# Kernel tuning notes

Hardware: AMD Instinct MI355X
Metric: run time of the kernel (lower is better)

## Reference

```python
import jax, jax.numpy as jnp
import numpy as np
from jax import lax

T, B, S = 64, 32, 64
V, E, H = 32000, 512, 512

def _p(key, shape, scale=0.05):
    return (jax.random.normal(key, shape, dtype=jnp.float32) * scale)

def setup_inputs() -> dict:
    key = jax.random.key(0)
    ks = jax.random.split(key, 24)
    inp = {
        'trg': jax.random.randint(ks[0], (T, B), 0, V),
        'encoded_src': jax.random.normal(ks[1], (S, B, 2 * H), dtype=jnp.float32),
        'emb': _p(ks[2], (V, E)),
        # LSTM layer 0: input = E + 2H
        'W_ih0': _p(ks[3], (4 * H, E + 2 * H)), 'W_hh0': _p(ks[4], (4 * H, H)),
        'b_ih0': _p(ks[5], (4 * H,)), 'b_hh0': _p(ks[6], (4 * H,)),
        # LSTM layer 1: input = H
        'W_ih1': _p(ks[7], (4 * H, H)), 'W_hh1': _p(ks[8], (4 * H, H)),
        'b_ih1': _p(ks[9], (4 * H,)), 'b_hh1': _p(ks[10], (4 * H,)),
        # attn_annot: 2H -> H
        'Wa': _p(ks[11], (H, 2 * H)), 'ba': _p(ks[12], (H,)),
        # attn_hidden: H -> H
        'Wh': _p(ks[13], (H, H)), 'bh': _p(ks[14], (H,)),
        # other: H -> 1
        'Wo': _p(ks[15], (1, H)), 'bo': _p(ks[16], (1,)),
        # penult: 3H -> E
        'Wp': _p(ks[17], (E, 3 * H)), 'bp': _p(ks[18], (E,)),
        # out bias (weight tied to emb)
        'b_out': _p(ks[19], (V,)),
    }
    return inp

def _lstm_cell(x, h, c, W_ih, W_hh, b_ih, b_hh):
    # PyTorch gate order: i, f, g, o
    g = x @ W_ih.T + b_ih + h @ W_hh.T + b_hh
    i, f, gg, o = jnp.split(g, 4, axis=-1)
    c_new = jax.nn.sigmoid(f) * c + jax.nn.sigmoid(i) * jnp.tanh(gg)
    h_new = jax.nn.sigmoid(o) * jnp.tanh(c_new)
    return h_new, c_new

def reference(trg, encoded_src, emb, W_ih0, W_hh0, b_ih0, b_hh0,
              W_ih1, W_hh1, b_ih1, b_hh1, Wa, ba, Wh, bh, Wo, bo,
              Wp, bp, b_out):
    trg_emb = emb[trg]                                # [T,B,E]
    annot_scores = encoded_src @ Wa.T + ba            # [S,B,H]
    Hd = W_hh0.shape[1]
    Bd = encoded_src.shape[1]
    h0 = jnp.zeros((2, Bd, Hd), dtype=encoded_src.dtype)
    c0 = jnp.zeros((2, Bd, Hd), dtype=encoded_src.dtype)
    ctx0 = jnp.zeros((Bd, encoded_src.shape[2]), dtype=encoded_src.dtype)

    def step(carry, emb_t):
        h, c, ctx = carry
        x = jnp.concatenate([emb_t, ctx], axis=1)      # [B, E+2H]
        h0n, c0n = _lstm_cell(x,   h[0], c[0], W_ih0, W_hh0, b_ih0, b_hh0)
        h1n, c1n = _lstm_cell(h0n, h[1], c[1], W_ih1, W_hh1, b_ih1, b_hh1)
        out = h1n                                      # [B,H]
        hs = out @ Wh.T + bh                           # [B,H]
        e = jnp.tanh(hs[None] + annot_scores) @ Wo.T + bo   # [S,B,1]
        a = jax.nn.softmax(e, axis=0)[..., 0]          # [S,B]
        ctx_new = jnp.einsum('sb,sbd->bd', a, encoded_src)  # [B,2H]
        stacked = jnp.concatenate([out, ctx_new], axis=1)   # [B,3H]
        return (jnp.stack([h0n, h1n]), jnp.stack([c0n, c1n]), ctx_new), stacked

    (h, c, _), all_scores = lax.scan(step, (h0, c0, ctx0), trg_emb)  # all_scores [T,B,3H]
    pen = all_scores @ Wp.T + bp                       # [T,B,E]
    logits = pen @ emb.T + b_out                       # [T,B,V] (tied weights)
    scores = jax.nn.log_softmax(logits, axis=2)
    return (scores, h, c)
```

## Files before the change

### kernel.cpp

```cpp
#include <hip/hip_runtime.h>


typedef unsigned short u16;
typedef short bf16x8 __attribute__((ext_vector_type(8)));
typedef float f32x4 __attribute__((ext_vector_type(4)));

#define MFMA_BF16(a, b, c) __builtin_amdgcn_mfma_f32_16x16x32_bf16((a), (b), (c), 0, 0, 0)

struct __attribute__((aligned(8))) U16x4 { u16 x, y, z, w; };

__device__ __forceinline__ float b2f(u16 u) {
  unsigned v = ((unsigned)u) << 16; float f; __builtin_memcpy(&f, &v, 4); return f;
}
__device__ __forceinline__ u16 f2b(float f) {
  unsigned u; __builtin_memcpy(&u, &f, 4);
  u = (u + 0x7FFFu + ((u >> 16) & 1u)) >> 16;
  return (u16)u;
}
__device__ __forceinline__ float sigm(float x) { return 1.f / (1.f + __expf(-x)); }
__device__ __forceinline__ float tanh_fast(float x) {
  x = fminf(fmaxf(x, -15.f), 15.f);
  float e = __expf(2.f * x);
  return (e - 1.f) / (e + 1.f);
}

__device__ __forceinline__ bf16x8 bl16(const u16* p) {
  bf16x8 v;
  asm volatile("global_load_dwordx4 %0, %1, off sc0 sc1" : "=v"(v) : "v"(p) : "memory");
  return v;
}
__device__ __forceinline__ float blf(const float* p) {
  float v;
  asm volatile("global_load_dword %0, %1, off sc0 sc1" : "=v"(v) : "v"(p) : "memory");
  return v;
}
__device__ __forceinline__ u16 blu16(const u16* p) {
  unsigned v;
  asm volatile("global_load_ushort %0, %1, off sc0 sc1" : "=v"(v) : "v"(p) : "memory");
  return (u16)v;
}
__device__ __forceinline__ void bs16(u16* p, u16 d) {
  unsigned dd = d;
  asm volatile("global_store_short %0, %1, off sc0 sc1" :: "v"(p), "v"(dd) : "memory");
}
__device__ __forceinline__ void bs32(float* p, float d) {
  asm volatile("global_store_dword %0, %1, off sc0 sc1" :: "v"(p), "v"(d) : "memory");
}
__device__ __forceinline__ void bs32u(u16* p, unsigned d) {
  asm volatile("global_store_dword %0, %1, off sc0 sc1" :: "v"(p), "v"(d) : "memory");
}
__device__ __forceinline__ void vmwait() {
  asm volatile("s_waitcnt vmcnt(0)" ::: "memory");
  __builtin_amdgcn_sched_barrier(0);
}

__global__ void f2b4_kernel(const float* __restrict__ src, u16* __restrict__ dst, long n4) {
  long i = (long)blockIdx.x * blockDim.x + threadIdx.x;
  long stride = (long)gridDim.x * blockDim.x;
  for (; i < n4; i += stride) {
    float4 v = ((const float4*)src)[i];
    U16x4 o; o.x = f2b(v.x); o.y = f2b(v.y); o.z = f2b(v.z); o.w = f2b(v.w);
    ((U16x4*)dst)[i] = o;
  }
}

__global__ void f2b4_strided(const float* __restrict__ src, u16* __restrict__ dst,
                             int rows, int cols4, int sld, int soff, int dld, int doff) {
  int total = rows * cols4;
  for (int i = blockIdx.x * blockDim.x + threadIdx.x; i < total; i += gridDim.x * blockDim.x) {
    int r = i / cols4, c4 = i - r * cols4;
    float4 v = *(const float4*)(src + (size_t)r * sld + soff + c4 * 4);
    U16x4 o; o.x = f2b(v.x); o.y = f2b(v.y); o.z = f2b(v.z); o.w = f2b(v.w);
    *(U16x4*)(dst + (size_t)r * dld + doff + c4 * 4) = o;
  }
}

__global__ void gather_emb_kernel(const int* __restrict__ trg, const float* __restrict__ emb,
                                  u16* __restrict__ out) {
  int r = blockIdx.x;
  int v = trg[r];
  const float* srow = emb + (size_t)v * 512;
  u16* drow = out + (size_t)r * 512;
  for (int e = threadIdx.x; e < 128; e += blockDim.x) {
    float4 x = ((const float4*)srow)[e];
    U16x4 o; o.x = f2b(x.x); o.y = f2b(x.y); o.z = f2b(x.z); o.w = f2b(x.w);
    ((U16x4*)drow)[e] = o;
  }
}

__global__ void annot_tr_kernel(const float* __restrict__ annot, u16* __restrict__ abt) {
  int b = blockIdx.x >> 6, s = blockIdx.x & 63;
  const float* src = annot + (size_t)(s * 32 + b) * 512;
  u16* dst = abt + (size_t)(b * 64 + s) * 512;
  int j = threadIdx.x;
  float4 v = ((const float4*)src)[j];
  U16x4 o; o.x = f2b(v.x); o.y = f2b(v.y); o.z = f2b(v.z); o.w = f2b(v.w);
  ((U16x4*)dst)[j] = o;
}

__global__ void enc_tr_kernel(const float* __restrict__ enc, u16* __restrict__ ebt) {
  int b = blockIdx.x >> 6, s = blockIdx.x & 63;
  const float* src = enc + (size_t)(s * 32 + b) * 1024;
  u16* dst = ebt + (size_t)(b * 64 + s) * 1024;
  int j = threadIdx.x;
  float4 v = ((const float4*)src)[j];
  U16x4 o; o.x = f2b(v.x); o.y = f2b(v.y); o.z = f2b(v.z); o.w = f2b(v.w);
  ((U16x4*)dst)[j] = o;
}

template <int MODE>
__global__ __launch_bounds__(256) void gemm_bt(
    const u16* __restrict__ A, const u16* __restrict__ B,
    float* __restrict__ outF, u16* __restrict__ outB,
    const float* __restrict__ bias0, const float* __restrict__ bias1,
    int N, int K, int ntiles, float* __restrict__ pmax, float* __restrict__ psum) {
  const int l = threadIdx.x & 63, wv = threadIdx.x >> 6;
  const int m0 = blockIdx.x * 128 + wv * 32;
  const int n0 = blockIdx.y * 64;
  const int kg = ((l >> 4) << 3);
  const u16* Ap0 = A + (size_t)(m0 + (l & 15)) * K + kg;
  const u16* Ap1 = Ap0 + (size_t)16 * K;
  const u16* Bp = B + (size_t)(n0 + (l & 15)) * K + kg;
  f32x4 acc[2][4] = {};
  for (int k0 = 0; k0 < K; k0 += 32) {
    bf16x8 a0 = *(const bf16x8*)(Ap0 + k0);
    bf16x8 a1 = *(const bf16x8*)(Ap1 + k0);
#pragma unroll
    for (int nf = 0; nf < 4; ++nf) {
      bf16x8 bb = *(const bf16x8*)(Bp + (size_t)(nf * 16) * K + k0);
      acc[0][nf] = MFMA_BF16(a0, bb, acc[0][nf]);
      acc[1][nf] = MFMA_BF16(a1, bb, acc[1][nf]);
    }
  }
  float biasv[4];
#pragma unroll
  for (int nf = 0; nf < 4; ++nf) {
    int col = n0 + nf * 16 + (l & 15);
    float bv = bias0 ? bias0[col] : 0.f;
    if (bias1) bv += bias1[col];
    biasv[nf] = bv;
  }
#pragma unroll
  for (int mi = 0; mi < 2; ++mi)
#pragma unroll
    for (int nf = 0; nf < 4; ++nf)
#pragma unroll
      for (int i = 0; i < 4; ++i) acc[mi][nf][i] += biasv[nf];

#pragma unroll
  for (int mi = 0; mi < 2; ++mi)
#pragma unroll
    for (int i = 0; i < 4; ++i) {
      int row = m0 + mi * 16 + ((l >> 4) << 2) + i;
#pragma unroll
      for (int nf = 0; nf < 4; ++nf) {
        int col = n0 + nf * 16 + (l & 15);
        if constexpr (MODE == 1)
          outB[(size_t)row * N + col] = f2b(acc[mi][nf][i]);
        else
          outF[(size_t)row * N + col] = acc[mi][nf][i];
      }
    }
  if constexpr (MODE == 2) {
    float lm[2][4], se[2][4];
#pragma unroll
    for (int mi = 0; mi < 2; ++mi)
#pragma unroll
      for (int i = 0; i < 4; ++i) {
        float m_ = acc[mi][0][i];
#pragma unroll
        for (int nf = 1; nf < 4; ++nf) m_ = fmaxf(m_, acc[mi][nf][i]);
        lm[mi][i] = m_;
      }
#pragma unroll
    for (int d = 1; d < 16; d <<= 1)
#pragma unroll
      for (int mi = 0; mi < 2; ++mi)
#pragma unroll
        for (int i = 0; i < 4; ++i) lm[mi][i] = fmaxf(lm[mi][i], __shfl_xor(lm[mi][i], d));
#pragma unroll
    for (int mi = 0; mi < 2; ++mi)
#pragma unroll
      for (int i = 0; i < 4; ++i) {
        float s_ = 0.f;
#pragma unroll
        for (int nf = 0; nf < 4; ++nf) s_ += __expf(acc[mi][nf][i] - lm[mi][i]);
        se[mi][i] = s_;
      }
#pragma unroll
    for (int d = 1; d < 16; d <<= 1)
#pragma unroll
      for (int mi = 0; mi < 2; ++mi)
#pragma unroll
        for (int i = 0; i < 4; ++i) se[mi][i] += __shfl_xor(se[mi][i], d);
    if ((l & 15) == 0) {
#pragma unroll
      for (int mi = 0; mi < 2; ++mi)
#pragma unroll
        for (int i = 0; i < 4; ++i) {
          int row = m0 + mi * 16 + ((l >> 4) << 2) + i;
          pmax[(size_t)row * ntiles + blockIdx.y] = lm[mi][i];
          psum[(size_t)row * ntiles + blockIdx.y] = se[mi][i];
        }
    }
  }
}

__device__ __forceinline__ void grid_barrier(unsigned* flags, unsigned phase) {
  __syncthreads();
  if (threadIdx.x == 0) {
    __hip_atomic_store(flags + blockIdx.x * 32, phase, __ATOMIC_RELAXED,
                       __HIP_MEMORY_SCOPE_AGENT);
  }
  if (threadIdx.x < 32) {
    int spins = 0;
    while (__hip_atomic_load(flags + threadIdx.x * 32, __ATOMIC_RELAXED,
                             __HIP_MEMORY_SCOPE_AGENT) < phase &&
           spins < 2000000) ++spins;
  }
  __syncthreads();
}

__global__ __launch_bounds__(512, 2) void scan_kernel(
    const u16* __restrict__ xW0,
    const u16* __restrict__ Wcat0,
    const u16* __restrict__ Wcat1,
    const u16* __restrict__ Whb,
    const float* __restrict__ b_ih1, const float* __restrict__ b_hh1,
    const float* __restrict__ bh, const float* __restrict__ Wo, const float* __restrict__ bo,
    const u16* __restrict__ annot_bt,
    const u16* __restrict__ enc_bt,
    u16* __restrict__ ctxb,
    u16* __restrict__ h0b,
    u16* __restrict__ h1b,
    float* __restrict__ c0, float* __restrict__ c1,
    float* __restrict__ hs,
    u16* __restrict__ scoresb,
    float* __restrict__ dout_hc,
    unsigned* __restrict__ flags) {
  __shared__ float sm[16384];
  const int w = blockIdx.x;
  const int tid = threadIdx.x;
  const int l = tid & 63, wv = tid >> 6;
  const int jh0 = w * 16;
  const int bE = tid >> 4, jlE = tid & 15;
  unsigned phase = 0;

  float gb1[4];
#pragma unroll
  for (int g = 0; g < 4; ++g) gb1[g] = b_ih1[g * 512 + jh0 + jlE] + b_hh1[g * 512 + jh0 + jlE];
  const float bhv = bh[jh0 + jlE];
  const float bov = bo[0];

  for (int t = 0; t < 64; ++t) {
    const int pA = t & 1;
    {
      const int kg = ((l >> 4) << 3);
      u16 xw[4];
      {
        const u16* xp = xW0 + (size_t)(t * 32 + bE) * 2048 + jh0 + jlE;
#pragma unroll
        for (int g = 0; g < 4; ++g) xw[g] = blu16(xp + g * 512);
      }
      bf16x8 a0[6], a1[6];
#pragma unroll
      for (int kk = 0; kk < 6; ++kk) {
        const int k0 = wv * 192 + kk * 32;
        const u16* ab; int ld, off;
        if (k0 < 1024) { ab = ctxb; ld = 1024; off = k0; }
        else { ab = h0b + pA * 32 * 512; ld = 512; off = k0 - 1024; }
        a0[kk] = bl16(ab + (size_t)(l & 15) * ld + off + kg);
        a1[kk] = bl16(ab + (size_t)((l & 15) + 16) * ld + off + kg);
      }
      vmwait();
      f32x4 acc[2][4] = {};
#pragma unroll
      for (int kk = 0; kk < 6; ++kk) {
        const int k0 = wv * 192 + kk * 32;
#pragma unroll
        for (int g = 0; g < 4; ++g) {
          bf16x8 bb = *(const bf16x8*)(Wcat0 + (size_t)(g * 512 + jh0 + (l & 15)) * 1536 + k0 + kg);
          acc[0][g] = MFMA_BF16(a0[kk], bb, acc[0][g]);
          acc[1][g] = MFMA_BF16(a1[kk], bb, acc[1][g]);
        }
      }
#pragma unroll
      for (int mi = 0; mi < 2; ++mi)
#pragma unroll
        for (int g = 0; g < 4; ++g)
#pragma unroll
          for (int i = 0; i < 4; ++i) {
            int m = mi * 16 + ((l >> 4) << 2) + i;
            sm[(wv * 32 + m) * 64 + g * 16 + (l & 15)] = acc[mi][g][i];
          }
      __syncthreads();
      {
        const int b = bE, jl = jlE, jh = jh0 + jl;
        float gate[4];
#pragma unroll
        for (int g = 0; g < 4; ++g) {
          float s = 0.f;
#pragma unroll
          for (int kv = 0; kv < 8; ++kv) s += sm[(kv * 32 + b) * 64 + g * 16 + jl];
          gate[g] = s + b2f(xw[g]);
        }
        float cn = sigm(gate[1]) * c0[b * 512 + jh] + sigm(gate[0]) * tanh_fast(gate[2]);
        float hn = sigm(gate[3]) * tanh_fast(cn);
        c0[b * 512 + jh] = cn;
        bs16(h0b + (pA ^ 1) * 32 * 512 + b * 512 + jh, f2b(hn));
        if (t == 63) { dout_hc[b * 512 + jh] = hn; dout_hc[32768 + b * 512 + jh] = cn; }
      }
    }
    grid_barrier(flags, ++phase);
    {
      const int kg = ((l >> 4) << 3);
      bf16x8 a0[4], a1[4];
#pragma unroll
      for (int kk = 0; kk < 4; ++kk) {
        const int k0 = wv * 128 + kk * 32;
        const u16* ab; int off;
        if (k0 < 512) { ab = h0b + (pA ^ 1) * 32 * 512; off = k0; }
        else { ab = h1b + pA * 32 * 512; off = k0 - 512; }
        a0[kk] = bl16(ab + (size_t)(l & 15) * 512 + off + kg);
        a1[kk] = bl16(ab + (size_t)((l & 15) + 16) * 512 + off + kg);
      }
      vmwait();
      f32x4 acc[2][4] = {};
#pragma unroll
      for (int kk = 0; kk < 4; ++kk) {
        const int k0 = wv * 128 + kk * 32;
#pragma unroll
        for (int g = 0; g < 4; ++g) {
          bf16x8 bb = *(const bf16x8*)(Wcat1 + (size_t)(g * 512 + jh0 + (l & 15)) * 1024 + k0 + kg);
          acc[0][g] = MFMA_BF16(a0[kk], bb, acc[0][g]);
          acc[1][g] = MFMA_BF16(a1[kk], bb, acc[1][g]);
        }
      }
#pragma unroll
      for (int mi = 0; mi < 2; ++mi)
#pragma unroll
        for (int g = 0; g < 4; ++g)
#pragma unroll
          for (int i = 0; i < 4; ++i) {
            int m = mi * 16 + ((l >> 4) << 2) + i;
            sm[(wv * 32 + m) * 64 + g * 16 + (l & 15)] = acc[mi][g][i];
          }
      __syncthreads();
      {
        const int b = bE, jl = jlE, jh = jh0 + jl;
        float gate[4];
#pragma unroll
        for (int g = 0; g < 4; ++g) {
          float s = 0.f;
#pragma unroll
          for (int kv = 0; kv < 8; ++kv) s += sm[(kv * 32 + b) * 64 + g * 16 + jl];
          gate[g] = s + gb1[g];
        }
        float cn = sigm(gate[1]) * c1[b * 512 + jh] + sigm(gate[0]) * tanh_fast(gate[2]);
        float hn = sigm(gate[3]) * tanh_fast(cn);
        c1[b * 512 + jh] = cn;
        u16 hb = f2b(hn);
        bs16(h1b + (pA ^ 1) * 32 * 512 + b * 512 + jh, hb);
        bs16(scoresb + (size_t)(t * 32 + b) * 1536 + jh, hb);
        if (t == 63) { dout_hc[16384 + b * 512 + jh] = hn; dout_hc[32768 + 16384 + b * 512 + jh] = cn; }
      }
    }
    grid_barrier(flags, ++phase);
    {
      const int kg = ((l >> 4) << 3);
      const u16* h1n = h1b + (pA ^ 1) * 32 * 512;
      bf16x8 a0[2], a1[2];
#pragma unroll
      for (int kk = 0; kk < 2; ++kk) {
        const int k0 = wv * 64 + kk * 32;
        a0[kk] = bl16(h1n + (size_t)(l & 15) * 512 + k0 + kg);
        a1[kk] = bl16(h1n + (size_t)((l & 15) + 16) * 512 + k0 + kg);
      }
      vmwait();
      f32x4 acc2[2] = {};
#pragma unroll
      for (int kk = 0; kk < 2; ++kk) {
        const int k0 = wv * 64 + kk * 32;
        bf16x8 bb = *(const bf16x8*)(Whb + (size_t)(jh0 + (l & 15)) * 512 + k0 + kg);
        acc2[0] = MFMA_BF16(a0[kk], bb, acc2[0]);
        acc2[1] = MFMA_BF16(a1[kk], bb, acc2[1]);
      }
#pragma unroll
      for (int mi = 0; mi < 2; ++mi)
#pragma unroll
        for (int i = 0; i < 4; ++i)
          sm[(wv * 32 + mi * 16 + ((l >> 4) << 2) + i) * 16 + (l & 15)] = acc2[mi][i];
      __syncthreads();
      {
        const int b = bE, jl = jlE;
        float s = 0.f;
#pragma unroll
        for (int kv = 0; kv < 8; ++kv) s += sm[(kv * 32 + b) * 16 + jl];
        bs32(hs + b * 512 + jh0 + jl, s + bhv);
      }
    }
    grid_barrier(flags, ++phase);
    {
      const int b = w;
      float* hs_s = sm;
      float* wo_s = sm + 512;
      float* red = sm + 1024;
      float* a_s = sm + 1536;
      float hv = blf(hs + b * 512 + tid);
      float wov = Wo[tid];
      vmwait();
      hs_s[tid] = hv;
      wo_s[tid] = wov;
      __syncthreads();
      const int s_ = tid >> 3, ks = tid & 7;
      const u16* arow = annot_bt + (size_t)(b * 64 + s_) * 512 + ks * 64;
      float accv = 0.f;
#pragma unroll
      for (int kk8 = 0; kk8 < 8; ++kk8) {
        bf16x8 av = *(const bf16x8*)(arow + kk8 * 8);
#pragma unroll
        for (int j = 0; j < 8; ++j) {
          int k = ks * 64 + kk8 * 8 + j;
          accv += tanh_fast(hs_s[k] + b2f((u16)av[j])) * wo_s[k];
        }
      }
      red[tid] = accv;
      __syncthreads();
      if (tid < 64) {
        float e = bov;
#pragma unroll
        for (int j = 0; j < 8; ++j) e += red[tid * 8 + j];
        float mx = e;
#pragma unroll
        for (int d = 1; d < 64; d <<= 1) mx = fmaxf(mx, __shfl_xor(mx, d));
        float p = __expf(e - mx);
        float ss = p;
#pragma unroll
        for (int d = 1; d < 64; d <<= 1) ss += __shfl_xor(ss, d);
        a_s[tid] = p / ss;
      }
      __syncthreads();
      float cx0 = 0.f, cx1 = 0.f;
      const u16* erow = enc_bt + (size_t)b * 65536 + tid * 2;
#pragma unroll 8
      for (int s2 = 0; s2 < 64; ++s2) {
        unsigned ev = *(const unsigned*)(erow + (size_t)s2 * 1024);
        float av = a_s[s2];
        cx0 += av * b2f((u16)(ev & 0xFFFFu));
        cx1 += av * b2f((u16)(ev >> 16));
      }
      u16 u0 = f2b(cx0), u1 = f2b(cx1);
      unsigned pk = (unsigned)u0 | ((unsigned)u1 << 16);
      bs32u(ctxb + b * 1024 + tid * 2, pk);
      bs32u(scoresb + (size_t)(t * 32 + b) * 1536 + 512 + tid * 2, pk);
    }
    grid_barrier(flags, ++phase);
  }
}

__global__ __launch_bounds__(256) void lse_kernel(const float* __restrict__ pmax,
                                                  const float* __restrict__ psum,
                                                  float* __restrict__ lse, int nt) {
  __shared__ float red[256];
  const int r = blockIdx.x;
  float m = -3.4e38f;
  for (int j = threadIdx.x; j < nt; j += 256) m = fmaxf(m, pmax[(size_t)r * nt + j]);
  red[threadIdx.x] = m; __syncthreads();
  for (int s = 128; s > 0; s >>= 1) {
    if (threadIdx.x < s) red[threadIdx.x] = fmaxf(red[threadIdx.x], red[threadIdx.x + s]);
    __syncthreads();
  }
  const float M = red[0]; __syncthreads();
  float s_ = 0.f;
  for (int j = threadIdx.x; j < nt; j += 256)
    s_ += psum[(size_t)r * nt + j] * __expf(pmax[(size_t)r * nt + j] - M);
  red[threadIdx.x] = s_; __syncthreads();
  for (int s = 128; s > 0; s >>= 1) {
    if (threadIdx.x < s) red[threadIdx.x] += red[threadIdx.x + s];
    __syncthreads();
  }
  if (threadIdx.x == 0) lse[r] = M + logf(red[0]);
}

__global__ void finalize_kernel(float* __restrict__ out, const float* __restrict__ lse) {
  const long n4 = 16384000;
  for (long i = (long)blockIdx.x * blockDim.x + threadIdx.x; i < n4;
       i += (long)gridDim.x * blockDim.x) {
    float4 v = ((float4*)out)[i];
    float L = lse[i / 8000];
    v.x -= L; v.y -= L; v.z -= L; v.w -= L;
    ((float4*)out)[i] = v;
  }
}

extern "C" void kernel_launch(void* const* d_in, const int* in_sizes, int n_in,
                              void* d_out, int out_size, void* d_ws, size_t ws_size,
                              hipStream_t stream) {
  const int* trg = (const int*)d_in[0];
  const float* enc = (const float*)d_in[1];
  const float* emb = (const float*)d_in[2];
  const float* W_ih0 = (const float*)d_in[3];
  const float* W_hh0 = (const float*)d_in[4];
  const float* b_ih0 = (const float*)d_in[5];
  const float* b_hh0 = (const float*)d_in[6];
  const float* W_ih1 = (const float*)d_in[7];
  const float* W_hh1 = (const float*)d_in[8];
  const float* b_ih1 = (const float*)d_in[9];
  const float* b_hh1 = (const float*)d_in[10];
  const float* Wa = (const float*)d_in[11];
  const float* ba = (const float*)d_in[12];
  const float* Wh = (const float*)d_in[13];
  const float* bh = (const float*)d_in[14];
  const float* Wo = (const float*)d_in[15];
  const float* bo = (const float*)d_in[16];
  const float* Wp = (const float*)d_in[17];
  const float* bp = (const float*)d_in[18];
  const float* b_out = (const float*)d_in[19];
  float* out = (float*)d_out;

  unsigned char* ws = (unsigned char*)d_ws;
  size_t off = 0;
  auto alloc = [&](size_t bytes) -> void* {
    void* p = ws + off; off += (bytes + 255) & ~(size_t)255; return p;
  };
  u16* emb_b = (u16*)alloc(32768000);
  u16* trgemb_b = (u16*)alloc(2097152);
  u16* enc_b = (u16*)alloc(4194304);
  u16* Wemb0_b = (u16*)alloc(2097152);
  u16* Wcat0_b = (u16*)alloc(6291456);
  u16* Wcat1_b = (u16*)alloc(4194304);
  u16* Wa_b = (u16*)alloc(1048576);
  u16* Wh_b = (u16*)alloc(524288);
  u16* Wp_b = (u16*)alloc(1572864);
  u16* xW0_b = (u16*)alloc(8388608);
  float* annot = (float*)alloc(4194304);
  u16* scoresb = (u16*)alloc(6291456);
  u16* pen_b = (u16*)alloc(2097152);
  u16* ctxb = (u16*)alloc(65536);
  u16* h0b = (u16*)alloc(65536);
  u16* h1b = (u16*)alloc(65536);
  float* c0 = (float*)alloc(65536);
  float* c1 = (float*)alloc(65536);
  float* hsbuf = (float*)alloc(65536);
  float* pmax = (float*)alloc(4194304);
  float* psum = (float*)alloc(4194304);
  float* lse = (float*)alloc(8192);
  unsigned* flags = (unsigned*)alloc(4096);
  if (off > ws_size) return;

  u16* annot_bt = (u16*)pmax;
  u16* enc_bt = (u16*)psum;

  hipMemsetAsync(ctxb, 0, 65536, stream);
  hipMemsetAsync(h0b, 0, 65536, stream);
  hipMemsetAsync(h1b, 0, 65536, stream);
  hipMemsetAsync(c0, 0, 65536, stream);
  hipMemsetAsync(c1, 0, 65536, stream);
  hipMemsetAsync(flags, 0, 4096, stream);

  f2b4_kernel<<<1024, 256, 0, stream>>>(emb, emb_b, 4096000);
  f2b4_kernel<<<256, 256, 0, stream>>>(enc, enc_b, 524288);
  f2b4_kernel<<<128, 256, 0, stream>>>(Wa, Wa_b, 131072);
  f2b4_kernel<<<64, 256, 0, stream>>>(Wh, Wh_b, 65536);
  f2b4_kernel<<<128, 256, 0, stream>>>(Wp, Wp_b, 196608);
  f2b4_strided<<<512, 256, 0, stream>>>(W_ih0, Wemb0_b, 2048, 128, 1536, 0, 512, 0);
  f2b4_strided<<<512, 256, 0, stream>>>(W_ih0, Wcat0_b, 2048, 256, 1536, 512, 1536, 0);
  f2b4_strided<<<512, 256, 0, stream>>>(W_hh0, Wcat0_b, 2048, 128, 512, 0, 1536, 1024);
  f2b4_strided<<<512, 256, 0, stream>>>(W_ih1, Wcat1_b, 2048, 128, 512, 0, 1024, 0);
  f2b4_strided<<<512, 256, 0, stream>>>(W_hh1, Wcat1_b, 2048, 128, 512, 0, 1024, 512);
  gather_emb_kernel<<<2048, 128, 0, stream>>>(trg, emb, trgemb_b);
  enc_tr_kernel<<<2048, 256, 0, stream>>>(enc, enc_bt);

  gemm_bt<1><<<dim3(16, 32), 256, 0, stream>>>(trgemb_b, Wemb0_b, nullptr, xW0_b,
                                               b_ih0, b_hh0, 2048, 512, 0, nullptr, nullptr);
  gemm_bt<0><<<dim3(16, 8), 256, 0, stream>>>(enc_b, Wa_b, annot, nullptr,
                                              ba, nullptr, 512, 1024, 0, nullptr, nullptr);
  annot_tr_kernel<<<2048, 128, 0, stream>>>(annot, annot_bt);

  scan_kernel<<<32, 512, 0, stream>>>(xW0_b, Wcat0_b, Wcat1_b, Wh_b, b_ih1, b_hh1, bh, Wo, bo,
                                      annot_bt, enc_bt, ctxb, h0b, h1b, c0, c1, hsbuf, scoresb,
                                      out + 65536000, flags);
  gemm_bt<1><<<dim3(16, 8), 256, 0, stream>>>(scoresb, Wp_b, nullptr, pen_b,
                                              bp, nullptr, 512, 1536, 0, nullptr, nullptr);
  gemm_bt<2><<<dim3(16, 500), 256, 0, stream>>>(pen_b, emb_b, out, nullptr,
                                                b_out, nullptr, 32000, 512, 500, pmax, psum);
  lse_kernel<<<2048, 256, 0, stream>>>(pmax, psum, lse, 500);
  finalize_kernel<<<2048, 256, 0, stream>>>(out, lse);
}
```

Baseline: 2.522 ms.

## Fuse attention-hidden projection into per-batch block, dropping one grid barrier per step

Result: slower. 3.408 ms (+35.1%).

```diff
diff --git a/kernel.cpp b/kernel.cpp
--- a/kernel.cpp
+++ b/kernel.cpp
@@ -29,22 +29,10 @@
   asm volatile("global_load_dwordx4 %0, %1, off sc0 sc1" : "=v"(v) : "v"(p) : "memory");
   return v;
 }
-__device__ __forceinline__ float blf(const float* p) {
-  float v;
-  asm volatile("global_load_dword %0, %1, off sc0 sc1" : "=v"(v) : "v"(p) : "memory");
-  return v;
-}
 __device__ __forceinline__ u16 blu16(const u16* p) {
   unsigned v;
   asm volatile("global_load_ushort %0, %1, off sc0 sc1" : "=v"(v) : "v"(p) : "memory");
   return (u16)v;
-}
-__device__ __forceinline__ void bs16(u16* p, u16 d) {
-  unsigned dd = d;
-  asm volatile("global_store_short %0, %1, off sc0 sc1" :: "v"(p), "v"(dd) : "memory");
-}
-__device__ __forceinline__ void bs32(float* p, float d) {
-  asm volatile("global_store_dword %0, %1, off sc0 sc1" :: "v"(p), "v"(d) : "memory");
 }
 __device__ __forceinline__ void bs32u(u16* p, unsigned d) {
   asm volatile("global_store_dword %0, %1, off sc0 sc1" :: "v"(p), "v"(d) : "memory");
@@ -221,7 +209,7 @@
   __syncthreads();
 }
 
-__global__ __launch_bounds__(512, 2) void scan_kernel(
+__global__ __launch_bounds__(512) void scan_kernel(
     const u16* __restrict__ xW0,
     const u16* __restrict__ Wcat0,
     const u16* __restrict__ Wcat1,
@@ -233,12 +221,12 @@
     u16* __restrict__ ctxb,
     u16* __restrict__ h0b,
     u16* __restrict__ h1b,
-    float* __restrict__ c0, float* __restrict__ c1,
-    float* __restrict__ hs,
     u16* __restrict__ scoresb,
     float* __restrict__ dout_hc,
     unsigned* __restrict__ flags) {
   __shared__ float sm[16384];
+  __shared__ float c0s[512];
+  __shared__ float c1s[512];
   const int w = blockIdx.x;
   const int tid = threadIdx.x;
   const int l = tid & 63, wv = tid >> 6;
@@ -246,29 +234,31 @@
   const int bE = tid >> 4, jlE = tid & 15;
   unsigned phase = 0;
 
+  c0s[tid] = 0.f; c1s[tid] = 0.f;
+
   float gb1[4];
 #pragma unroll
   for (int g = 0; g < 4; ++g) gb1[g] = b_ih1[g * 512 + jh0 + jlE] + b_hh1[g * 512 + jh0 + jlE];
-  const float bhv = bh[jh0 + jlE];
   const float bov = bo[0];
+
+  u16 xw_cur[4];
+  {
+    const u16* xp = xW0 + (size_t)(0 * 32 + bE) * 2048 + jh0 + jlE;
+#pragma unroll
+    for (int g = 0; g < 4; ++g) xw_cur[g] = blu16(xp + g * 512);
+  }
 
   for (int t = 0; t < 64; ++t) {
     const int pA = t & 1;
     {
       const int kg = ((l >> 4) << 3);
-      u16 xw[4];
-      {
-        const u16* xp = xW0 + (size_t)(t * 32 + bE) * 2048 + jh0 + jlE;
-#pragma unroll
-        for (int g = 0; g < 4; ++g) xw[g] = blu16(xp + g * 512);
-      }
       bf16x8 a0[6], a1[6];
 #pragma unroll
       for (int kk = 0; kk < 6; ++kk) {
         const int k0 = wv * 192 + kk * 32;
         const u16* ab; int ld, off;
         if (k0 < 1024) { ab = ctxb; ld = 1024; off = k0; }
-        else { ab = h0b + pA * 32 * 512; ld = 512; off = k0 - 1024; }
+        else { ab = h0b + pA * 16384; ld = 512; off = k0 - 1024; }
         a0[kk] = bl16(ab + (size_t)(l & 15) * ld + off + kg);
         a1[kk] = bl16(ab + (size_t)((l & 15) + 16) * ld + off + kg);
       }
@@ -291,23 +281,27 @@
 #pragma unroll
           for (int i = 0; i < 4; ++i) {
             int m = mi * 16 + ((l >> 4) << 2) + i;
-            sm[(wv * 32 + m) * 64 + g * 16 + (l & 15)] = acc[mi][g][i];
+            sm[wv * 2048 + m * 64 + ((g * 16 + (l & 15)) ^ (i << 3))] = acc[mi][g][i];
           }
       __syncthreads();
       {
         const int b = bE, jl = jlE, jh = jh0 + jl;
+        const int cxb = (b & 3) << 3;
         float gate[4];
 #pragma unroll
         for (int g = 0; g < 4; ++g) {
+          const int cx = b * 64 + ((g * 16 + jl) ^ cxb);
           float s = 0.f;
 #pragma unroll
-          for (int kv = 0; kv < 8; ++kv) s += sm[(kv * 32 + b) * 64 + g * 16 + jl];
-          gate[g] = s + b2f(xw[g]);
-        }
-        float cn = sigm(gate[1]) * c0[b * 512 + jh] + sigm(gate[0]) * tanh_fast(gate[2]);
+          for (int kv = 0; kv < 8; ++kv) s += sm[kv * 2048 + cx];
+          gate[g] = s + b2f(xw_cur[g]);
+        }
+        float cn = sigm(gate[1]) * c0s[tid] + sigm(gate[0]) * tanh_fast(gate[2]);
         float hn = sigm(gate[3]) * tanh_fast(cn);
-        c0[b * 512 + jh] = cn;
-        bs16(h0b + (pA ^ 1) * 32 * 512 + b * 512 + jh, f2b(hn));
+        c0s[tid] = cn;
+        unsigned hb = f2b(hn);
+        unsigned hi = __shfl_down(hb, 1);
+        if ((jl & 1) == 0) bs32u(h0b + (pA ^ 1) * 16384 + b * 512 + jh, hb | (hi << 16));
         if (t == 63) { dout_hc[b * 512 + jh] = hn; dout_hc[32768 + b * 512 + jh] = cn; }
       }
     }
@@ -319,8 +313,8 @@
       for (int kk = 0; kk < 4; ++kk) {
         const int k0 = wv * 128 + kk * 32;
         const u16* ab; int off;
-        if (k0 < 512) { ab = h0b + (pA ^ 1) * 32 * 512; off = k0; }
-        else { ab = h1b + pA * 32 * 512; off = k0 - 512; }
+        if (k0 < 512) { ab = h0b + (pA ^ 1) * 16384; off = k0; }
+        else { ab = h1b + pA * 16384; off = k0 - 512; }
         a0[kk] = bl16(ab + (size_t)(l & 15) * 512 + off + kg);
         a1[kk] = bl16(ab + (size_t)((l & 15) + 16) * 512 + off + kg);
       }
@@ -343,74 +337,74 @@
 #pragma unroll
           for (int i = 0; i < 4; ++i) {
             int m = mi * 16 + ((l >> 4) << 2) + i;
-            sm[(wv * 32 + m) * 64 + g * 16 + (l & 15)] = acc[mi][g][i];
+            sm[wv * 2048 + m * 64 + ((g * 16 + (l & 15)) ^ (i << 3))] = acc[mi][g][i];
           }
       __syncthreads();
       {
         const int b = bE, jl = jlE, jh = jh0 + jl;
+        const int cxb = (b & 3) << 3;
         float gate[4];
 #pragma unroll
         for (int g = 0; g < 4; ++g) {
+          const int cx = b * 64 + ((g * 16 + jl) ^ cxb);
           float s = 0.f;
 #pragma unroll
-          for (int kv = 0; kv < 8; ++kv) s += sm[(kv * 32 + b) * 64 + g * 16 + jl];
+          for (int kv = 0; kv < 8; ++kv) s += sm[kv * 2048 + cx];
           gate[g] = s + gb1[g];
         }
-        float cn = sigm(gate[1]) * c1[b * 512 + jh] + sigm(gate[0]) * tanh_fast(gate[2]);
+        float cn = sigm(gate[1]) * c1s[tid] + sigm(gate[0]) * tanh_fast(gate[2]);
         float hn = sigm(gate[3]) * tanh_fast(cn);
-        c1[b * 512 + jh] = cn;
-        u16 hb = f2b(hn);
-        bs16(h1b + (pA ^ 1) * 32 * 512 + b * 512 + jh, hb);
-        bs16(scoresb + (size_t)(t * 32 + b) * 1536 + jh, hb);
-        if (t == 63) { dout_hc[16384 + b * 512 + jh] = hn; dout_hc[32768 + 16384 + b * 512 + jh] = cn; }
-      }
-    }
-    grid_barrier(flags, ++phase);
-    {
-      const int kg = ((l >> 4) << 3);
-      const u16* h1n = h1b + (pA ^ 1) * 32 * 512;
-      bf16x8 a0[2], a1[2];
-#pragma unroll
-      for (int kk = 0; kk < 2; ++kk) {
-        const int k0 = wv * 64 + kk * 32;
-        a0[kk] = bl16(h1n + (size_t)(l & 15) * 512 + k0 + kg);
-        a1[kk] = bl16(h1n + (size_t)((l & 15) + 16) * 512 + k0 + kg);
-      }
-      vmwait();
-      f32x4 acc2[2] = {};
-#pragma unroll
-      for (int kk = 0; kk < 2; ++kk) {
-        const int k0 = wv * 64 + kk * 32;
-        bf16x8 bb = *(const bf16x8*)(Whb + (size_t)(jh0 + (l & 15)) * 512 + k0 + kg);
-        acc2[0] = MFMA_BF16(a0[kk], bb, acc2[0]);
-        acc2[1] = MFMA_BF16(a1[kk], bb, acc2[1]);
-      }
-#pragma unroll
-      for (int mi = 0; mi < 2; ++mi)
-#pragma unroll
-        for (int i = 0; i < 4; ++i)
-          sm[(wv * 32 + mi * 16 + ((l >> 4) << 2) + i) * 16 + (l & 15)] = acc2[mi][i];
-      __syncthreads();
-      {
-        const int b = bE, jl = jlE;
-        float s = 0.f;
-#pragma unroll
-        for (int kv = 0; kv < 8; ++kv) s += sm[(kv * 32 + b) * 16 + jl];
-        bs32(hs + b * 512 + jh0 + jl, s + bhv);
+        c1s[tid] = cn;
+        unsigned hb = f2b(hn);
+        unsigned hi = __shfl_down(hb, 1);
+        if ((jl & 1) == 0) {
+          unsigned pk = hb | (hi << 16);
+          bs32u(h1b + (pA ^ 1) * 16384 + b * 512 + jh, pk);
+          bs32u(scoresb + (size_t)(t * 32 + b) * 1536 + jh, pk);
+        }
+        if (t == 63) { dout_hc[16384 + b * 512 + jh] = hn; dout_hc[49152 + b * 512 + jh] = cn; }
       }
     }
     grid_barrier(flags, ++phase);
     {
       const int b = w;
-      float* hs_s = sm;
-      float* wo_s = sm + 512;
-      float* red = sm + 1024;
-      float* a_s = sm + 1536;
-      float hv = blf(hs + b * 512 + tid);
+      u16* h1_sb = (u16*)sm;
+      float* hs_s = sm + 256;
+      float* wo_s = sm + 768;
+      float* red  = sm + 1280;
+      float* a_s  = sm + 1792;
+      u16 hv = blu16(h1b + (pA ^ 1) * 16384 + b * 512 + tid);
       float wov = Wo[tid];
+      {
+        int tn = (t + 1) & 63;
+        const u16* xp = xW0 + (size_t)(tn * 32 + bE) * 2048 + jh0 + jlE;
+#pragma unroll
+        for (int g = 0; g < 4; ++g) xw_cur[g] = blu16(xp + g * 512);
+      }
       vmwait();
-      hs_s[tid] = hv;
+      h1_sb[tid] = hv;
       wo_s[tid] = wov;
+      __syncthreads();
+      {
+        const int kg = ((l >> 4) << 3);
+        f32x4 acc2[4] = {};
+#pragma unroll
+        for (int kk = 0; kk < 16; ++kk) {
+          bf16x8 av = *(const bf16x8*)(h1_sb + kk * 32 + kg);
+#pragma unroll
+          for (int nf = 0; nf < 4; ++nf) {
+            bf16x8 bb = *(const bf16x8*)(Whb + (size_t)(wv * 64 + nf * 16 + (l & 15)) * 512 + kk * 32 + kg);
+            acc2[nf] = MFMA_BF16(av, bb, acc2[nf]);
+          }
+        }
+        if (l < 16) {
+#pragma unroll
+          for (int nf = 0; nf < 4; ++nf) {
+            int n = wv * 64 + nf * 16 + l;
+            hs_s[n] = acc2[nf][0] + bh[n];
+          }
+        }
+      }
       __syncthreads();
       const int s_ = tid >> 3, ks = tid & 7;
       const u16* arow = annot_bt + (size_t)(b * 64 + s_) * 512 + ks * 64;
@@ -449,8 +443,7 @@
         cx0 += av * b2f((u16)(ev & 0xFFFFu));
         cx1 += av * b2f((u16)(ev >> 16));
       }
-      u16 u0 = f2b(cx0), u1 = f2b(cx1);
-      unsigned pk = (unsigned)u0 | ((unsigned)u1 << 16);
+      unsigned pk = (unsigned)f2b(cx0) | ((unsigned)f2b(cx1) << 16);
       bs32u(ctxb + b * 1024 + tid * 2, pk);
       bs32u(scoresb + (size_t)(t * 32 + b) * 1536 + 512 + tid * 2, pk);
     }
@@ -539,9 +532,6 @@
   u16* ctxb = (u16*)alloc(65536);
   u16* h0b = (u16*)alloc(65536);
   u16* h1b = (u16*)alloc(65536);
-  float* c0 = (float*)alloc(65536);
-  float* c1 = (float*)alloc(65536);
-  float* hsbuf = (float*)alloc(65536);
   float* pmax = (float*)alloc(4194304);
   float* psum = (float*)alloc(4194304);
   float* lse = (float*)alloc(8192);
@@ -554,8 +544,6 @@
   hipMemsetAsync(ctxb, 0, 65536, stream);
   hipMemsetAsync(h0b, 0, 65536, stream);
   hipMemsetAsync(h1b, 0, 65536, stream);
-  hipMemsetAsync(c0, 0, 65536, stream);
-  hipMemsetAsync(c1, 0, 65536, stream);
   hipMemsetAsync(flags, 0, 4096, stream);
 
   f2b4_kernel<<<1024, 256, 0, stream>>>(emb, emb_b, 4096000);
@@ -578,7 +566,7 @@
   annot_tr_kernel<<<2048, 128, 0, stream>>>(annot, annot_bt);
 
   scan_kernel<<<32, 512, 0, stream>>>(xW0_b, Wcat0_b, Wcat1_b, Wh_b, b_ih1, b_hh1, bh, Wo, bo,
-                                      annot_bt, enc_bt, ctxb, h0b, h1b, c0, c1, hsbuf, scoresb,
+                                      annot_bt, enc_bt, ctxb, h0b, h1b, scoresb,
                                       out + 65536000, flags);
   gemm_bt<1><<<dim3(16, 8), 256, 0, stream>>>(scoresb, Wp_b, nullptr, pen_b,
                                               bp, nullptr, 512, 1536, 0, nullptr, nullptr);
```

## Split batch into two halves with per-half flag sync to pipeline scan phases

Applied to the files above, without the earlier changes.

New measurement: 3.312 ms. 1.31x slower.

```diff
diff --git a/kernel.cpp b/kernel.cpp
--- a/kernel.cpp
+++ b/kernel.cpp
@@ -39,14 +39,10 @@
   asm volatile("global_load_ushort %0, %1, off sc0 sc1" : "=v"(v) : "v"(p) : "memory");
   return (u16)v;
 }
-__device__ __forceinline__ void bs16(u16* p, u16 d) {
-  unsigned dd = d;
-  asm volatile("global_store_short %0, %1, off sc0 sc1" :: "v"(p), "v"(dd) : "memory");
-}
-__device__ __forceinline__ void bs32(float* p, float d) {
+__device__ __forceinline__ void bs32u(u16* p, unsigned d) {
   asm volatile("global_store_dword %0, %1, off sc0 sc1" :: "v"(p), "v"(d) : "memory");
 }
-__device__ __forceinline__ void bs32u(u16* p, unsigned d) {
+__device__ __forceinline__ void bsf32(float* p, float d) {
   asm volatile("global_store_dword %0, %1, off sc0 sc1" :: "v"(p), "v"(d) : "memory");
 }
 __device__ __forceinline__ void vmwait() {
@@ -206,19 +202,37 @@
   }
 }
 
-__device__ __forceinline__ void grid_barrier(unsigned* flags, unsigned phase) {
-  __syncthreads();
-  if (threadIdx.x == 0) {
-    __hip_atomic_store(flags + blockIdx.x * 32, phase, __ATOMIC_RELAXED,
-                       __HIP_MEMORY_SCOPE_AGENT);
-  }
+__device__ __forceinline__ void waitPh(unsigned* flags, int g, unsigned val) {
   if (threadIdx.x < 32) {
     int spins = 0;
-    while (__hip_atomic_load(flags + threadIdx.x * 32, __ATOMIC_RELAXED,
-                             __HIP_MEMORY_SCOPE_AGENT) < phase &&
-           spins < 2000000) ++spins;
+    while (__hip_atomic_load(flags + (size_t)(g * 32 + (int)threadIdx.x) * 32,
+                             __ATOMIC_RELAXED, __HIP_MEMORY_SCOPE_AGENT) < val &&
+           spins < 4000000) ++spins;
   }
   __syncthreads();
+}
+__device__ __forceinline__ void waitC2f(unsigned* flags, int g, unsigned val) {
+  if (threadIdx.x < 16) {
+    int spins = 0;
+    while (__hip_atomic_load(flags + 2048 + (size_t)(g * 16 + (int)threadIdx.x) * 32,
+                             __ATOMIC_RELAXED, __HIP_MEMORY_SCOPE_AGENT) < val &&
+           spins < 4000000) ++spins;
+  }
+  __syncthreads();
+}
+__device__ __forceinline__ void pubPh(unsigned* flags, int g, int w, unsigned val) {
+  vmwait();
+  __syncthreads();
+  if (threadIdx.x == 0)
+    __hip_atomic_store(flags + (size_t)(g * 32 + w) * 32, val,
+                       __ATOMIC_RELAXED, __HIP_MEMORY_SCOPE_AGENT);
+}
+__device__ __forceinline__ void pubC2(unsigned* flags, int g, int b16, unsigned val) {
+  vmwait();
+  __syncthreads();
+  if (threadIdx.x == 0)
+    __hip_atomic_store(flags + 2048 + (size_t)(g * 16 + b16) * 32, val,
+                       __ATOMIC_RELAXED, __HIP_MEMORY_SCOPE_AGENT);
 }
 
 __global__ __launch_bounds__(512, 2) void scan_kernel(
@@ -233,187 +247,215 @@
     u16* __restrict__ ctxb,
     u16* __restrict__ h0b,
     u16* __restrict__ h1b,
-    float* __restrict__ c0, float* __restrict__ c1,
     float* __restrict__ hs,
     u16* __restrict__ scoresb,
     float* __restrict__ dout_hc,
     unsigned* __restrict__ flags) {
-  __shared__ float sm[16384];
-  const int w = blockIdx.x;
-  const int tid = threadIdx.x;
+  __shared__ float sm[8192];
+  __shared__ float c0s[512], c1s[512];
+  const int w = blockIdx.x, tid = threadIdx.x;
   const int l = tid & 63, wv = tid >> 6;
   const int jh0 = w * 16;
-  const int bE = tid >> 4, jlE = tid & 15;
-  unsigned phase = 0;
+  const int hOwn = w >> 4;
+  const int b16E = tid >> 4, jlE = tid & 15;
+
+  c0s[tid] = 0.f; c1s[tid] = 0.f;
 
   float gb1[4];
 #pragma unroll
-  for (int g = 0; g < 4; ++g) gb1[g] = b_ih1[g * 512 + jh0 + jlE] + b_hh1[g * 512 + jh0 + jlE];
+  for (int q = 0; q < 4; ++q)
+    gb1[q] = b_ih1[q * 512 + jh0 + jlE] + b_hh1[q * 512 + jh0 + jlE];
   const float bhv = bh[jh0 + jlE];
   const float bov = bo[0];
 
+  unsigned xw[2][4];
+  if (tid < 256) {
+#pragma unroll
+    for (int g = 0; g < 2; ++g) {
+      const u16* xp = xW0 + (size_t)(g * 16 + b16E) * 2048 + jh0 + jlE;
+#pragma unroll
+      for (int q = 0; q < 4; ++q) xw[g][q] = blu16(xp + q * 512);
+    }
+  }
+
   for (int t = 0; t < 64; ++t) {
     const int pA = t & 1;
-    {
-      const int kg = ((l >> 4) << 3);
-      u16 xw[4];
-      {
-        const u16* xp = xW0 + (size_t)(t * 32 + bE) * 2048 + jh0 + jlE;
-#pragma unroll
-        for (int g = 0; g < 4; ++g) xw[g] = blu16(xp + g * 512);
-      }
-      bf16x8 a0[6], a1[6];
+    const unsigned ph1v = 3 * t + 1, ph2v = 3 * t + 2, ph3v = 3 * t + 3;
+
+#pragma unroll
+    for (int g = 0; g < 2; ++g) {
+      waitC2f(flags, g, (unsigned)t);
+      const int kg = (l >> 4) << 3;
+      bf16x8 a0[6];
 #pragma unroll
       for (int kk = 0; kk < 6; ++kk) {
         const int k0 = wv * 192 + kk * 32;
-        const u16* ab; int ld, off;
-        if (k0 < 1024) { ab = ctxb; ld = 1024; off = k0; }
-        else { ab = h0b + pA * 32 * 512; ld = 512; off = k0 - 1024; }
-        a0[kk] = bl16(ab + (size_t)(l & 15) * ld + off + kg);
-        a1[kk] = bl16(ab + (size_t)((l & 15) + 16) * ld + off + kg);
+        const u16* p;
+        if (k0 < 1024) p = ctxb + g * 16384 + (size_t)(l & 15) * 1024 + k0 + kg;
+        else p = h0b + g * 16384 + pA * 8192 + (size_t)(l & 15) * 512 + (k0 - 1024) + kg;
+        a0[kk] = bl16(p);
       }
       vmwait();
-      f32x4 acc[2][4] = {};
+      f32x4 acc[4] = {};
 #pragma unroll
       for (int kk = 0; kk < 6; ++kk) {
         const int k0 = wv * 192 + kk * 32;
 #pragma unroll
-        for (int g = 0; g < 4; ++g) {
-          bf16x8 bb = *(const bf16x8*)(Wcat0 + (size_t)(g * 512 + jh0 + (l & 15)) * 1536 + k0 + kg);
-          acc[0][g] = MFMA_BF16(a0[kk], bb, acc[0][g]);
-          acc[1][g] = MFMA_BF16(a1[kk], bb, acc[1][g]);
-        }
-      }
-#pragma unroll
-      for (int mi = 0; mi < 2; ++mi)
-#pragma unroll
-        for (int g = 0; g < 4; ++g)
-#pragma unroll
-          for (int i = 0; i < 4; ++i) {
-            int m = mi * 16 + ((l >> 4) << 2) + i;
-            sm[(wv * 32 + m) * 64 + g * 16 + (l & 15)] = acc[mi][g][i];
-          }
+        for (int q = 0; q < 4; ++q) {
+          bf16x8 bb = *(const bf16x8*)(Wcat0 + (size_t)(q * 512 + jh0 + (l & 15)) * 1536 + k0 + kg);
+          acc[q] = MFMA_BF16(a0[kk], bb, acc[q]);
+        }
+      }
+#pragma unroll
+      for (int q = 0; q < 4; ++q)
+#pragma unroll
+        for (int i = 0; i < 4; ++i) {
+          int m = ((l >> 4) << 2) + i;
+          int key = ((m ^ (m >> 2)) & 3) << 3;
+          sm[wv * 1024 + m * 64 + ((q * 16 + (l & 15)) ^ key)] = acc[q][i];
+        }
       __syncthreads();
-      {
-        const int b = bE, jl = jlE, jh = jh0 + jl;
+      if (tid < 256) {
+        const int b16 = b16E, jl = jlE, jh = jh0 + jl;
+        const int key = ((b16 ^ (b16 >> 2)) & 3) << 3;
         float gate[4];
 #pragma unroll
-        for (int g = 0; g < 4; ++g) {
+        for (int q = 0; q < 4; ++q) {
+          const int cx = b16 * 64 + ((q * 16 + jl) ^ key);
           float s = 0.f;
 #pragma unroll
-          for (int kv = 0; kv < 8; ++kv) s += sm[(kv * 32 + b) * 64 + g * 16 + jl];
-          gate[g] = s + b2f(xw[g]);
-        }
-        float cn = sigm(gate[1]) * c0[b * 512 + jh] + sigm(gate[0]) * tanh_fast(gate[2]);
+          for (int kv = 0; kv < 8; ++kv) s += sm[kv * 1024 + cx];
+          gate[q] = s + b2f((u16)xw[g][q]);
+        }
+        float cn = sigm(gate[1]) * c0s[g * 256 + tid] + sigm(gate[0]) * tanh_fast(gate[2]);
         float hn = sigm(gate[3]) * tanh_fast(cn);
-        c0[b * 512 + jh] = cn;
-        bs16(h0b + (pA ^ 1) * 32 * 512 + b * 512 + jh, f2b(hn));
-        if (t == 63) { dout_hc[b * 512 + jh] = hn; dout_hc[32768 + b * 512 + jh] = cn; }
-      }
-    }
-    grid_barrier(flags, ++phase);
-    {
-      const int kg = ((l >> 4) << 3);
-      bf16x8 a0[4], a1[4];
+        c0s[g * 256 + tid] = cn;
+        unsigned hb = f2b(hn);
+        unsigned hi2 = __shfl_down(hb, 1);
+        if (!(jl & 1)) bs32u(h0b + g * 16384 + (pA ^ 1) * 8192 + b16 * 512 + jh, hb | (hi2 << 16));
+        if (t == 63) {
+          int ba = g * 16 + b16;
+          dout_hc[ba * 512 + jh] = hn; dout_hc[32768 + ba * 512 + jh] = cn;
+        }
+      }
+      pubPh(flags, g, w, ph1v);
+    }
+
+#pragma unroll
+    for (int g = 0; g < 2; ++g) {
+      waitPh(flags, g, ph1v);
+      const int kg = (l >> 4) << 3;
+      bf16x8 a0[4];
 #pragma unroll
       for (int kk = 0; kk < 4; ++kk) {
         const int k0 = wv * 128 + kk * 32;
-        const u16* ab; int off;
-        if (k0 < 512) { ab = h0b + (pA ^ 1) * 32 * 512; off = k0; }
-        else { ab = h1b + pA * 32 * 512; off = k0 - 512; }
-        a0[kk] = bl16(ab + (size_t)(l & 15) * 512 + off + kg);
-        a1[kk] = bl16(ab + (size_t)((l & 15) + 16) * 512 + off + kg);
+        const u16* p;
+        if (k0 < 512) p = h0b + g * 16384 + (pA ^ 1) * 8192 + (size_t)(l & 15) * 512 + k0 + kg;
+        else p = h1b + g * 16384 + pA * 8192 + (size_t)(l & 15) * 512 + (k0 - 512) + kg;
+        a0[kk] = bl16(p);
       }
       vmwait();
-      f32x4 acc[2][4] = {};
+      f32x4 acc[4] = {};
 #pragma unroll
       for (int kk = 0; kk < 4; ++kk) {
         const int k0 = wv * 128 + kk * 32;
 #pragma unroll
-        for (int g = 0; g < 4; ++g) {
-          bf16x8 bb = *(const bf16x8*)(Wcat1 + (size_t)(g * 512 + jh0 + (l & 15)) * 1024 + k0 + kg);
-          acc[0][g] = MFMA_BF16(a0[kk], bb, acc[0][g]);
-          acc[1][g] = MFMA_BF16(a1[kk], bb, acc[1][g]);
-        }
-      }
-#pragma unroll
-      for (int mi = 0; mi < 2; ++mi)
-#pragma unroll
-        for (int g = 0; g < 4; ++g)
-#pragma unroll
-          for (int i = 0; i < 4; ++i) {
-            int m = mi * 16 + ((l >> 4) << 2) + i;
-            sm[(wv * 32 + m) * 64 + g * 16 + (l & 15)] = acc[mi][g][i];
-          }
+        for (int q = 0; q < 4; ++q) {
+          bf16x8 bb = *(const bf16x8*)(Wcat1 + (size_t)(q * 512 + jh0 + (l & 15)) * 1024 + k0 + kg);
+          acc[q] = MFMA_BF16(a0[kk], bb, acc[q]);
+        }
+      }
+#pragma unroll
+      for (int q = 0; q < 4; ++q)
+#pragma unroll
+        for (int i = 0; i < 4; ++i) {
+          int m = ((l >> 4) << 2) + i;
+          int key = ((m ^ (m >> 2)) & 3) << 3;
+          sm[wv * 1024 + m * 64 + ((q * 16 + (l & 15)) ^ key)] = acc[q][i];
+        }
       __syncthreads();
-      {
-        const int b = bE, jl = jlE, jh = jh0 + jl;
+      if (tid < 256) {
+        const int b16 = b16E, jl = jlE, jh = jh0 + jl;
+        const int key = ((b16 ^ (b16 >> 2)) & 3) << 3;
         float gate[4];
 #pragma unroll
-        for (int g = 0; g < 4; ++g) {
+        for (int q = 0; q < 4; ++q) {
+          const int cx = b16 * 64 + ((q * 16 + jl) ^ key);
           float s = 0.f;
 #pragma unroll
-          for (int kv = 0; kv < 8; ++kv) s += sm[(kv * 32 + b) * 64 + g * 16 + jl];
-          gate[g] = s + gb1[g];
-        }
-        float cn = sigm(gate[1]) * c1[b * 512 + jh] + sigm(gate[0]) * tanh_fast(gate[2]);
+          for (int kv = 0; kv < 8; ++kv) s += sm[kv * 1024 + cx];
+          gate[q] = s + gb1[q];
+        }
+        float cn = sigm(gate[1]) * c1s[g * 256 + tid] + sigm(gate[0]) * tanh_fast(gate[2]);
         float hn = sigm(gate[3]) * tanh_fast(cn);
-        c1[b * 512 + jh] = cn;
-        u16 hb = f2b(hn);
-        bs16(h1b + (pA ^ 1) * 32 * 512 + b * 512 + jh, hb);
-        bs16(scoresb + (size_t)(t * 32 + b) * 1536 + jh, hb);
-        if (t == 63) { dout_hc[16384 + b * 512 + jh] = hn; dout_hc[32768 + 16384 + b * 512 + jh] = cn; }
-      }
-    }
-    grid_barrier(flags, ++phase);
-    {
-      const int kg = ((l >> 4) << 3);
-      const u16* h1n = h1b + (pA ^ 1) * 32 * 512;
-      bf16x8 a0[2], a1[2];
+        c1s[g * 256 + tid] = cn;
+        unsigned hb = f2b(hn);
+        unsigned hi2 = __shfl_down(hb, 1);
+        if (!(jl & 1)) {
+          unsigned pk = hb | (hi2 << 16);
+          bs32u(h1b + g * 16384 + (pA ^ 1) * 8192 + b16 * 512 + jh, pk);
+          bs32u(scoresb + (size_t)(t * 32 + g * 16 + b16) * 1536 + jh, pk);
+        }
+        if (t == 63) {
+          int ba = g * 16 + b16;
+          dout_hc[16384 + ba * 512 + jh] = hn; dout_hc[49152 + ba * 512 + jh] = cn;
+        }
+      }
+      pubPh(flags, g, w, ph2v);
+    }
+
+#pragma unroll
+    for (int g = 0; g < 2; ++g) {
+      waitPh(flags, g, ph2v);
+      if (tid < 256) {
+        const int tn = (t + 1) & 63;
+        const u16* xp = xW0 + (size_t)(tn * 32 + g * 16 + b16E) * 2048 + jh0 + jlE;
+#pragma unroll
+        for (int q = 0; q < 4; ++q) xw[g][q] = blu16(xp + q * 512);
+      }
+      const int kg = (l >> 4) << 3;
+      bf16x8 a0[2];
 #pragma unroll
       for (int kk = 0; kk < 2; ++kk) {
         const int k0 = wv * 64 + kk * 32;
-        a0[kk] = bl16(h1n + (size_t)(l & 15) * 512 + k0 + kg);
-        a1[kk] = bl16(h1n + (size_t)((l & 15) + 16) * 512 + k0 + kg);
+        a0[kk] = bl16(h1b + g * 16384 + (pA ^ 1) * 8192 + (size_t)(l & 15) * 512 + k0 + kg);
       }
       vmwait();
-      f32x4 acc2[2] = {};
+      f32x4 acc2 = {};
 #pragma unroll
       for (int kk = 0; kk < 2; ++kk) {
         const int k0 = wv * 64 + kk * 32;
         bf16x8 bb = *(const bf16x8*)(Whb + (size_t)(jh0 + (l & 15)) * 512 + k0 + kg);
-        acc2[0] = MFMA_BF16(a0[kk], bb, acc2[0]);
-        acc2[1] = MFMA_BF16(a1[kk], bb, acc2[1]);
-      }
-#pragma unroll
-      for (int mi = 0; mi < 2; ++mi)
-#pragma unroll
-        for (int i = 0; i < 4; ++i)
-          sm[(wv * 32 + mi * 16 + ((l >> 4) << 2) + i) * 16 + (l & 15)] = acc2[mi][i];
+        acc2 = MFMA_BF16(a0[kk], bb, acc2);
+      }
+#pragma unroll
+      for (int i = 0; i < 4; ++i)
+        sm[wv * 256 + (((l >> 4) << 2) + i) * 16 + (l & 15)] = acc2[i];
       __syncthreads();
-      {
-        const int b = bE, jl = jlE;
+      if (tid < 256) {
         float s = 0.f;
 #pragma unroll
-        for (int kv = 0; kv < 8; ++kv) s += sm[(kv * 32 + b) * 16 + jl];
-        bs32(hs + b * 512 + jh0 + jl, s + bhv);
-      }
-    }
-    grid_barrier(flags, ++phase);
+        for (int kv = 0; kv < 8; ++kv) s += sm[kv * 256 + b16E * 16 + jlE];
+        bsf32(hs + g * 8192 + b16E * 512 + jh0 + jlE, s + bhv);
+      }
+      pubPh(flags, g, w, ph3v);
+    }
+
     {
-      const int b = w;
+      waitPh(flags, hOwn, ph3v);
+      const int b16 = w & 15, ba = w;
       float* hs_s = sm;
       float* wo_s = sm + 512;
-      float* red = sm + 1024;
-      float* a_s = sm + 1536;
-      float hv = blf(hs + b * 512 + tid);
+      float* red  = sm + 1024;
+      float* a_s  = sm + 1536;
+      float hv = blf(hs + hOwn * 8192 + b16 * 512 + tid);
       float wov = Wo[tid];
       vmwait();
       hs_s[tid] = hv;
       wo_s[tid] = wov;
       __syncthreads();
       const int s_ = tid >> 3, ks = tid & 7;
-      const u16* arow = annot_bt + (size_t)(b * 64 + s_) * 512 + ks * 64;
+      const u16* arow = annot_bt + (size_t)(ba * 64 + s_) * 512 + ks * 64;
       float accv = 0.f;
 #pragma unroll
       for (int kk8 = 0; kk8 < 8; ++kk8) {
@@ -441,7 +483,7 @@
       }
       __syncthreads();
       float cx0 = 0.f, cx1 = 0.f;
-      const u16* erow = enc_bt + (size_t)b * 65536 + tid * 2;
+      const u16* erow = enc_bt + (size_t)ba * 65536 + tid * 2;
 #pragma unroll 8
       for (int s2 = 0; s2 < 64; ++s2) {
         unsigned ev = *(const unsigned*)(erow + (size_t)s2 * 1024);
@@ -449,12 +491,11 @@
         cx0 += av * b2f((u16)(ev & 0xFFFFu));
         cx1 += av * b2f((u16)(ev >> 16));
       }
-      u16 u0 = f2b(cx0), u1 = f2b(cx1);
-      unsigned pk = (unsigned)u0 | ((unsigned)u1 << 16);
-      bs32u(ctxb + b * 1024 + tid * 2, pk);
-      bs32u(scoresb + (size_t)(t * 32 + b) * 1536 + 512 + tid * 2, pk);
-    }
-    grid_barrier(flags, ++phase);
+      unsigned pk = (unsigned)f2b(cx0) | ((unsigned)f2b(cx1) << 16);
+      bs32u(ctxb + hOwn * 16384 + b16 * 1024 + tid * 2, pk);
+      bs32u(scoresb + (size_t)(t * 32 + ba) * 1536 + 512 + tid * 2, pk);
+      pubC2(flags, hOwn, b16, (unsigned)(t + 1));
+    }
   }
 }
 
@@ -539,13 +580,11 @@
   u16* ctxb = (u16*)alloc(65536);
   u16* h0b = (u16*)alloc(65536);
   u16* h1b = (u16*)alloc(65536);
-  float* c0 = (float*)alloc(65536);
-  float* c1 = (float*)alloc(65536);
   float* hsbuf = (float*)alloc(65536);
   float* pmax = (float*)alloc(4194304);
   float* psum = (float*)alloc(4194304);
   float* lse = (float*)alloc(8192);
-  unsigned* flags = (unsigned*)alloc(4096);
+  unsigned* flags = (unsigned*)alloc(16384);
   if (off > ws_size) return;
 
   u16* annot_bt = (u16*)pmax;
@@ -554,9 +593,7 @@
   hipMemsetAsync(ctxb, 0, 65536, stream);
   hipMemsetAsync(h0b, 0, 65536, stream);
   hipMemsetAsync(h1b, 0, 65536, stream);
-  hipMemsetAsync(c0, 0, 65536, stream);
-  hipMemsetAsync(c1, 0, 65536, stream);
-  hipMemsetAsync(flags, 0, 4096, stream);
+  hipMemsetAsync(flags, 0, 16384, stream);
 
   f2b4_kernel<<<1024, 256, 0, stream>>>(emb, emb_b, 4096000);
   f2b4_kernel<<<256, 256, 0, stream>>>(enc, enc_b, 524288);
@@ -578,7 +615,7 @@
   annot_tr_kernel<<<2048, 128, 0, stream>>>(annot, annot_bt);
 
   scan_kernel<<<32, 512, 0, stream>>>(xW0_b, Wcat0_b, Wcat1_b, Wh_b, b_ih1, b_hh1, bh, Wo, bo,
-                                      annot_bt, enc_bt, ctxb, h0b, h1b, c0, c1, hsbuf, scoresb,
+                                      annot_bt, enc_bt, ctxb, h0b, h1b, hsbuf, scoresb,
                                       out + 65536000, flags);
   gemm_bt<1><<<dim3(16, 8), 256, 0, stream>>>(scoresb, Wp_b, nullptr, pen_b,
                                               bp, nullptr, 512, 1536, 0, nullptr, nullptr);
```
